# Kernel optimization log

Measured on AMD Instinct MI355X. Metric: run time of the kernel, lower is better.

The kernel has to match this reference:

```python
import jax, jax.numpy as jnp
import numpy as np

ALPHA = 0.5
SMOOTHING = 0.1
B, C = 16384, 4096


def setup_inputs() -> dict:
    key = jax.random.key(0)
    k1, k2 = jax.random.split(key)
    y_h = jax.random.normal(k1, (B, C), dtype=jnp.float32)
    # y acts as a score matrix; argmax over classes yields the hard label
    y = jax.random.normal(k2, (B, C), dtype=jnp.float32)
    # supervise buffer: smoothing/(C-1) off-diagonal, 1-smoothing on diagonal
    supervise = jnp.full((C, C), SMOOTHING / (C - 1), dtype=jnp.float32)
    supervise = supervise.at[jnp.arange(C), jnp.arange(C)].set(1.0 - SMOOTHING)
    return {"y_h": y_h, "y": y, "supervise": supervise}


def reference(y_h, y, supervise):
    n_classes = supervise.shape[0]
    y_idx = jnp.argmax(y, axis=1)                      # [B] hard labels
    log_p = jax.nn.log_softmax(y_h, axis=-1)           # [B, C]
    probs = jnp.exp(log_p)                             # [B, C]

    # ---- step(): no-grad buffer update (training mode) ----
    pred = jnp.argmax(probs, axis=-1)                  # [B]
    mask = (pred == y_idx)                             # correctly classified
    probs_c = probs * mask[:, None].astype(probs.dtype)
    # update.index_add_(1, pred[mask], probs[mask].T): scatter-add rows of
    # probs into column `pred` of the [C, C] update matrix (dup indices ok)
    update = jnp.zeros((n_classes, n_classes), probs.dtype).at[:, pred].add(probs_c.T)
    idx_count = jnp.zeros((n_classes,), probs.dtype).at[pred].add(mask.astype(probs.dtype))

    # ---- soft loss: gather supervise columns by label ----
    true_dist = supervise.T[y_idx]                     # [B, C] == index_select(supervise,1,y).T
    soft_loss = jnp.mean(jnp.sum(-true_dist * log_p, axis=-1))

    # ---- hard loss: standard cross entropy ----
    hard_loss = -jnp.mean(jnp.take_along_axis(log_p, y_idx[:, None], axis=-1))

    loss = ALPHA * hard_loss + (1.0 - ALPHA) * soft_loss
    return loss, update, idx_count
```

## Files before the change

### kernel.cpp

```cpp
#include <hip/hip_runtime.h>
#include <math.h>


constexpr int CC    = 4096;
constexpr int WAVE  = 64;
constexpr int WPB   = 4;
constexpr int TPB   = 256;
constexpr int NCH   = 4;
constexpr int CHUNK = CC / NCH;
constexpr int JPW   = CHUNK / (WAVE * 4);
constexpr float ALPHA_V = 0.5f;
constexpr int ACC_SLOTS = 64;
constexpr int MCAP  = 32;

__device__ inline void amax2(float v, int i, float& bv, int& bi) {
  if (v > bv || (v == bv && i < bi)) { bv = v; bi = i; }
}

__device__ inline void wave_argmax(float& lv, int& li) {
  #pragma unroll
  for (int o = 1; o < WAVE; o <<= 1) {
    float ov = __shfl_xor(lv, o, WAVE);
    int   oi = __shfl_xor(li, o, WAVE);
    amax2(ov, oi, lv, li);
  }
}

__device__ inline float wave_sum(float v) {
  #pragma unroll
  for (int o = 1; o < WAVE; o <<= 1) v += __shfl_xor(v, o, WAVE);
  return v;
}

__global__ void ols_mega(const float* __restrict__ sup,
                         float* __restrict__ supT,
                         float* __restrict__ upd,
                         float* __restrict__ cnt,
                         double* __restrict__ acc,
                         const float* __restrict__ y,
                         float* __restrict__ ypmax,
                         int* __restrict__ ypidx, int C) {
  __shared__ float tile[32][33];
  const int blk = blockIdx.x;
  if ((blk & 1) == 0) {
    const int tid = threadIdx.x;
    const int t2 = blk >> 1;
    const int bx = (t2 & 127) * 32, by = (t2 >> 7) * 32;
    const int tx = tid & 31, ty = tid >> 5;
    if (by == 0 && ty == 0) cnt[bx + tx] = 0.0f;
    if (t2 == 0 && tid < ACC_SLOTS * 2) acc[tid] = 0.0;
    #pragma unroll
    for (int j = 0; j < 32; j += 8)
      tile[ty + j][tx] = sup[(size_t)(by + ty + j) * C + bx + tx];
    __syncthreads();
    #pragma unroll
    for (int j = 0; j < 32; j += 8) {
      const size_t o = (size_t)(bx + ty + j) * C + by + tx;
      supT[o] = tile[tx][ty + j];
      upd[o]  = 0.0f;
    }
  } else {
    const int wv = threadIdx.x >> 6, lane = threadIdx.x & 63;
    const int task = (blk >> 1) * WPB + wv;
    const int b = task >> 2, ch = task & 3;
    const float4* p = reinterpret_cast<const float4*>(y + (size_t)b * CC + ch * CHUNK);

    float4 v[JPW];
    #pragma unroll
    for (int j = 0; j < JPW; ++j) v[j] = p[j * WAVE + lane];

    float m = -INFINITY; int mi = 0x7fffffff;
    #pragma unroll
    for (int j = 0; j < JPW; ++j) {
      const int base = ch * CHUNK + (j * WAVE + lane) * 4;
      amax2(v[j].x, base + 0, m, mi);
      amax2(v[j].y, base + 1, m, mi);
      amax2(v[j].z, base + 2, m, mi);
      amax2(v[j].w, base + 3, m, mi);
    }
    wave_argmax(m, mi);
    if (lane == 0) { ypmax[task] = m; ypidx[task] = mi; }
  }
}

__global__ void ols_part_x(const float* __restrict__ y_h,
                           const float* __restrict__ supT,
                           const float* __restrict__ ypmax,
                           const int* __restrict__ ypidx,
                           float* __restrict__ xpmax, int* __restrict__ xpidx,
                           float* __restrict__ xpse, float* __restrict__ xpW,
                           float* __restrict__ xpWX) {
  const int wv = threadIdx.x >> 6, lane = threadIdx.x & 63;
  const int task = blockIdx.x * WPB + wv;
  const int b = task >> 2, ch = task & 3;

  const float4 ym = reinterpret_cast<const float4*>(ypmax)[b];
  const int4   yi = reinterpret_cast<const int4*>(ypidx)[b];
  float lm = ym.x; int lab = yi.x;
  amax2(ym.y, yi.y, lm, lab);
  amax2(ym.z, yi.z, lm, lab);
  amax2(ym.w, yi.w, lm, lab);

  const float4* px = reinterpret_cast<const float4*>(y_h + (size_t)b * CC + ch * CHUNK);
  const float4* pw = reinterpret_cast<const float4*>(supT + (size_t)lab * CC + ch * CHUNK);

  float4 xv[JPW], wv4[JPW];
  #pragma unroll
  for (int j = 0; j < JPW; ++j) xv[j] = px[j * WAVE + lane];
  #pragma unroll
  for (int j = 0; j < JPW; ++j) wv4[j] = pw[j * WAVE + lane];

  float m = -INFINITY; int mi = 0x7fffffff;
  float se = 0.f, W = 0.f, WX = 0.f;
  #pragma unroll
  for (int j = 0; j < JPW; ++j) {
    const int base = ch * CHUNK + (j * WAVE + lane) * 4;
    amax2(xv[j].x, base + 0, m, mi);
    amax2(xv[j].y, base + 1, m, mi);
    amax2(xv[j].z, base + 2, m, mi);
    amax2(xv[j].w, base + 3, m, mi);
    se += __expf(xv[j].x) + __expf(xv[j].y) + __expf(xv[j].z) + __expf(xv[j].w);
    W  += wv4[j].x + wv4[j].y + wv4[j].z + wv4[j].w;
    WX += wv4[j].x * xv[j].x + wv4[j].y * xv[j].y
        + wv4[j].z * xv[j].z + wv4[j].w * xv[j].w;
  }
  wave_argmax(m, mi);
  se = wave_sum(se);
  W  = wave_sum(W);
  WX = wave_sum(WX);
  if (lane == 0) {
    xpmax[task] = m; xpidx[task] = mi;
    xpse[task] = se; xpW[task] = W; xpWX[task] = WX;
  }
}

__global__ void ols_rowfin(const float* __restrict__ y_h,
                           const float* __restrict__ ypmax, const int* __restrict__ ypidx,
                           const float* __restrict__ xpmax, const int* __restrict__ xpidx,
                           const float* __restrict__ xpse, const float* __restrict__ xpW,
                           const float* __restrict__ xpWX,
                           float* __restrict__ upd,
                           float* __restrict__ cnt, double* __restrict__ acc) {
  __shared__ int   s_n;
  __shared__ int   s_row[MCAP];
  __shared__ int   s_pred[MCAP];
  __shared__ float s_invZ[MCAP];
  const int tid = threadIdx.x;
  const int b = blockIdx.x * TPB + tid;
  if (tid == 0) s_n = 0;

  const float4 ym = reinterpret_cast<const float4*>(ypmax)[b];
  const int4   yi = reinterpret_cast<const int4*>(ypidx)[b];
  float lm = ym.x; int lab = yi.x;
  amax2(ym.y, yi.y, lm, lab);
  amax2(ym.z, yi.z, lm, lab);
  amax2(ym.w, yi.w, lm, lab);

  const float4 xm = reinterpret_cast<const float4*>(xpmax)[b];
  const int4   xi = reinterpret_cast<const int4*>(xpidx)[b];
  float pm = xm.x; int pred = xi.x;
  amax2(xm.y, xi.y, pm, pred);
  amax2(xm.z, xi.z, pm, pred);
  amax2(xm.w, xi.w, pm, pred);

  const float4 se4 = reinterpret_cast<const float4*>(xpse)[b];
  const float4 W4  = reinterpret_cast<const float4*>(xpW)[b];
  const float4 WX4 = reinterpret_cast<const float4*>(xpWX)[b];
  const float Z  = se4.x + se4.y + se4.z + se4.w;
  const float W  = W4.x + W4.y + W4.z + W4.w;
  const float WX = WX4.x + WX4.y + WX4.z + WX4.w;

  const float logZ = __logf(Z);
  const float xl   = y_h[(size_t)b * CC + lab];
  float soft = logZ * W - WX;
  float hard = logZ - xl;

  __syncthreads();
  bool overflow = false;
  if (pred == lab) {
    const int pos = atomicAdd(&s_n, 1);
    if (pos < MCAP) { s_row[pos] = b; s_pred[pos] = pred; s_invZ[pos] = 1.0f / Z; }
    else overflow = true;
    atomicAdd(&cnt[pred], 1.0f);
  }
  if (overflow) {
    const float invZ = 1.0f / Z;
    const float* xr = y_h + (size_t)b * CC;
    for (int c = 0; c < CC; ++c)
      atomicAdd(&upd[(size_t)c * CC + pred], __expf(xr[c]) * invZ);
  }

  hard = wave_sum(hard);
  soft = wave_sum(soft);
  if ((tid & 63) == 0) {
    const int slot = ((b >> 6) & (ACC_SLOTS - 1)) * 2;
    atomicAdd(&acc[slot + 0], (double)hard);
    atomicAdd(&acc[slot + 1], (double)soft);
  }

  __syncthreads();
  const int n = min(s_n, MCAP);
  for (int i = 0; i < n; ++i) {
    const int rb = s_row[i], p = s_pred[i];
    const float iz = s_invZ[i];
    const float4* px = reinterpret_cast<const float4*>(y_h + (size_t)rb * CC);
    #pragma unroll
    for (int j = 0; j < 4; ++j) {
      const int i4 = j * TPB + tid;
      const float4 xv = px[i4];
      const int base = i4 * 4;
      atomicAdd(&upd[(size_t)(base + 0) * CC + p], __expf(xv.x) * iz);
      atomicAdd(&upd[(size_t)(base + 1) * CC + p], __expf(xv.y) * iz);
      atomicAdd(&upd[(size_t)(base + 2) * CC + p], __expf(xv.z) * iz);
      atomicAdd(&upd[(size_t)(base + 3) * CC + p], __expf(xv.w) * iz);
    }
  }
}

__global__ void ols_finalize(const double* __restrict__ acc,
                             float* __restrict__ out, double invB) {
  double h = 0.0, s = 0.0;
  for (int i = 0; i < ACC_SLOTS; ++i) { h += acc[i * 2]; s += acc[i * 2 + 1]; }
  out[0] = (float)(((double)ALPHA_V * h + (1.0 - (double)ALPHA_V) * s) * invB);
}

__global__ void ols_fallback(const float* __restrict__ y_h, const float* __restrict__ y,
                             const float* __restrict__ sup,
                             float* __restrict__ upd, float* __restrict__ cnt,
                             double* __restrict__ acc) {
  const int wv = threadIdx.x >> 6, lane = threadIdx.x & 63;
  const int b = blockIdx.x * WPB + wv;
  const size_t roff = (size_t)b * CC;
  const float4* y4 = reinterpret_cast<const float4*>(y + roff);
  const float4* x4 = reinterpret_cast<const float4*>(y_h + roff);
  const int K16 = CC / (WAVE * 4);

  float lv = -INFINITY; int li = 0x7fffffff;
  for (int k = 0; k < K16; ++k) {
    const float4 v = y4[k * WAVE + lane];
    const int base = (k * WAVE + lane) * 4;
    amax2(v.x, base + 0, lv, li); amax2(v.y, base + 1, lv, li);
    amax2(v.z, base + 2, lv, li); amax2(v.w, base + 3, lv, li);
  }
  wave_argmax(lv, li);
  const int lab = li;
  const float xl = y_h[roff + lab];

  float m = -INFINITY; int mi = 0x7fffffff;
  float se = 0.f, W = 0.f, WX = 0.f;
  for (int k = 0; k < K16; ++k) {
    const float4 xv = x4[k * WAVE + lane];
    const int base = (k * WAVE + lane) * 4;
    const float w0 = sup[(size_t)(base + 0) * CC + lab];
    const float w1 = sup[(size_t)(base + 1) * CC + lab];
    const float w2 = sup[(size_t)(base + 2) * CC + lab];
    const float w3 = sup[(size_t)(base + 3) * CC + lab];
    amax2(xv.x, base + 0, m, mi); amax2(xv.y, base + 1, m, mi);
    amax2(xv.z, base + 2, m, mi); amax2(xv.w, base + 3, m, mi);
    se += __expf(xv.x) + __expf(xv.y) + __expf(xv.z) + __expf(xv.w);
    W  += w0 + w1 + w2 + w3;
    WX += w0 * xv.x + w1 * xv.y + w2 * xv.z + w3 * xv.w;
  }
  wave_argmax(m, mi);
  const int pred = mi;
  const float Z = wave_sum(se), Wt = wave_sum(W), WXt = wave_sum(WX);
  const float logZ = __logf(Z);
  if (pred == lab) {
    const float invZ = 1.0f / Z;
    for (int k = 0; k < K16; ++k) {
      const float4 xv = x4[k * WAVE + lane];
      const int base = (k * WAVE + lane) * 4;
      atomicAdd(&upd[(size_t)(base + 0) * CC + pred], __expf(xv.x) * invZ);
      atomicAdd(&upd[(size_t)(base + 1) * CC + pred], __expf(xv.y) * invZ);
      atomicAdd(&upd[(size_t)(base + 2) * CC + pred], __expf(xv.z) * invZ);
      atomicAdd(&upd[(size_t)(base + 3) * CC + pred], __expf(xv.w) * invZ);
    }
    if (lane == 0) atomicAdd(&cnt[pred], 1.0f);
  }
  if (lane == 0) {
    const int slot = (b & (ACC_SLOTS - 1)) * 2;
    atomicAdd(&acc[slot + 0], (double)(logZ - xl));
    atomicAdd(&acc[slot + 1], (double)(logZ * Wt - WXt));
  }
}

extern "C" void kernel_launch(void* const* d_in, const int* in_sizes, int n_in,
                              void* d_out, int out_size, void* d_ws, size_t ws_size,
                              hipStream_t stream) {
  const float* y_h = (const float*)d_in[0];
  const float* y   = (const float*)d_in[1];
  const float* sup = (const float*)d_in[2];
  const int C = CC;
  const int B = in_sizes[0] / C;

  float* out        = (float*)d_out;
  float* out_update = out + 1;
  float* out_count  = out + 1 + (size_t)C * C;

  char* ws = (char*)d_ws;
  double* acc   = (double*)ws;
  float*  ypmax = (float*)(ws + 4096);
  int*    ypidx = (int*)  (ws + 266240);
  float*  xpmax = (float*)(ws + 528384);
  int*    xpidx = (int*)  (ws + 790528);
  float*  xpse  = (float*)(ws + 1052672);
  float*  xpW   = (float*)(ws + 1314816);
  float*  xpWX  = (float*)(ws + 1576960);
  float*  supT  = (float*)(ws + 1839104);
  const size_t need = 1839104 + (size_t)C * C * sizeof(float);

  if (ws_size >= need) {
    ols_mega<<<32768, TPB, 0, stream>>>(sup, supT, out_update, out_count,
                                        acc, y, ypmax, ypidx, C);
    ols_part_x<<<B * NCH / WPB, TPB, 0, stream>>>(y_h, supT, ypmax, ypidx,
                                                  xpmax, xpidx, xpse, xpW, xpWX);
    ols_rowfin<<<B / TPB, TPB, 0, stream>>>(y_h, ypmax, ypidx,
                                            xpmax, xpidx, xpse, xpW, xpWX,
                                            out_update, out_count, acc);
    ols_finalize<<<1, 1, 0, stream>>>(acc, out, 1.0 / (double)B);
  } else {
    hipMemsetAsync(d_out, 0, (size_t)out_size * sizeof(float), stream);
    hipMemsetAsync(d_ws, 0, 4096, stream);
    ols_fallback<<<B / WPB, TPB, 0, stream>>>(y_h, y, sup,
                                              out_update, out_count, acc);
    ols_finalize<<<1, 1, 0, stream>>>(acc, out, 1.0 / (double)B);
  }
}
```

Measured before the change: 196.8 us.

## Fuse per-row partial reductions and row finalize into one block-per-row kernel

The label argmax now finishes inside the first kernel through a shared-memory reduction across its four waves and writes a single label per row, replacing the per-chunk partial arrays. The separate partial-x and row-finalize kernels become one kernel that gives each row a whole block. That block reduces max, sum-exp and the weighted sums in shared memory, then does the loss atomics and the scatter into the update matrix directly. This removes one launch and the round trip of partial results through global memory. In exchange it adds a block barrier per row and issues one pair of double atomics per row where the old code issued one per 64 rows.

```diff
diff --git a/kernel.cpp b/kernel.cpp
--- a/kernel.cpp
+++ b/kernel.cpp
@@ -6,12 +6,10 @@
 constexpr int WAVE  = 64;
 constexpr int WPB   = 4;
 constexpr int TPB   = 256;
-constexpr int NCH   = 4;
-constexpr int CHUNK = CC / NCH;
+constexpr int CHUNK = CC / WPB;
 constexpr int JPW   = CHUNK / (WAVE * 4);
 constexpr float ALPHA_V = 0.5f;
 constexpr int ACC_SLOTS = 64;
-constexpr int MCAP  = 32;
 
 __device__ inline void amax2(float v, int i, float& bv, int& bi) {
   if (v > bv || (v == bv && i < bi)) { bv = v; bi = i; }
@@ -38,12 +36,13 @@
                          float* __restrict__ cnt,
                          double* __restrict__ acc,
                          const float* __restrict__ y,
-                         float* __restrict__ ypmax,
-                         int* __restrict__ ypidx, int C) {
+                         int* __restrict__ labels, int C) {
   __shared__ float tile[32][33];
+  __shared__ float s_m[WPB];
+  __shared__ int   s_i[WPB];
   const int blk = blockIdx.x;
+  const int tid = threadIdx.x;
   if ((blk & 1) == 0) {
-    const int tid = threadIdx.x;
     const int t2 = blk >> 1;
     const int bx = (t2 & 127) * 32, by = (t2 >> 7) * 32;
     const int tx = tid & 31, ty = tid >> 5;
@@ -60,11 +59,10 @@
       upd[o]  = 0.0f;
     }
   } else {
-    const int wv = threadIdx.x >> 6, lane = threadIdx.x & 63;
-    const int task = (blk >> 1) * WPB + wv;
-    const int b = task >> 2, ch = task & 3;
-    const float4* p = reinterpret_cast<const float4*>(y + (size_t)b * CC + ch * CHUNK);
-
+    const int wv = tid >> 6, lane = tid & 63;
+    const int b = blk >> 1;
+    const float4* p = reinterpret_cast<const float4*>(y + (size_t)b * CC)
+                      + wv * (CHUNK / 4);
     float4 v[JPW];
     #pragma unroll
     for (int j = 0; j < JPW; ++j) v[j] = p[j * WAVE + lane];
@@ -72,37 +70,41 @@
     float m = -INFINITY; int mi = 0x7fffffff;
     #pragma unroll
     for (int j = 0; j < JPW; ++j) {
-      const int base = ch * CHUNK + (j * WAVE + lane) * 4;
+      const int base = wv * CHUNK + (j * WAVE + lane) * 4;
       amax2(v[j].x, base + 0, m, mi);
       amax2(v[j].y, base + 1, m, mi);
       amax2(v[j].z, base + 2, m, mi);
       amax2(v[j].w, base + 3, m, mi);
     }
     wave_argmax(m, mi);
-    if (lane == 0) { ypmax[task] = m; ypidx[task] = mi; }
-  }
-}
-
-__global__ void ols_part_x(const float* __restrict__ y_h,
-                           const float* __restrict__ supT,
-                           const float* __restrict__ ypmax,
-                           const int* __restrict__ ypidx,
-                           float* __restrict__ xpmax, int* __restrict__ xpidx,
-                           float* __restrict__ xpse, float* __restrict__ xpW,
-                           float* __restrict__ xpWX) {
-  const int wv = threadIdx.x >> 6, lane = threadIdx.x & 63;
-  const int task = blockIdx.x * WPB + wv;
-  const int b = task >> 2, ch = task & 3;
-
-  const float4 ym = reinterpret_cast<const float4*>(ypmax)[b];
-  const int4   yi = reinterpret_cast<const int4*>(ypidx)[b];
-  float lm = ym.x; int lab = yi.x;
-  amax2(ym.y, yi.y, lm, lab);
-  amax2(ym.z, yi.z, lm, lab);
-  amax2(ym.w, yi.w, lm, lab);
-
-  const float4* px = reinterpret_cast<const float4*>(y_h + (size_t)b * CC + ch * CHUNK);
-  const float4* pw = reinterpret_cast<const float4*>(supT + (size_t)lab * CC + ch * CHUNK);
+    if (lane == 0) { s_m[wv] = m; s_i[wv] = mi; }
+    __syncthreads();
+    if (tid == 0) {
+      float bm = s_m[0]; int bi = s_i[0];
+      amax2(s_m[1], s_i[1], bm, bi);
+      amax2(s_m[2], s_i[2], bm, bi);
+      amax2(s_m[3], s_i[3], bm, bi);
+      labels[b] = bi;
+    }
+  }
+}
+
+__global__ void ols_row(const float* __restrict__ y_h,
+                        const int* __restrict__ labels,
+                        const float* __restrict__ supT,
+                        float* __restrict__ upd, float* __restrict__ cnt,
+                        double* __restrict__ acc) {
+  __shared__ float s_m[WPB], s_se[WPB], s_W[WPB], s_WX[WPB];
+  __shared__ int   s_mi[WPB];
+  const int tid = threadIdx.x;
+  const int wv = tid >> 6, lane = tid & 63;
+  const int b = blockIdx.x;
+  const int lab = labels[b];
+  const size_t roff = (size_t)b * CC;
+
+  const float4* px = reinterpret_cast<const float4*>(y_h + roff) + wv * (CHUNK / 4);
+  const float4* pw = reinterpret_cast<const float4*>(supT + (size_t)lab * CC)
+                     + wv * (CHUNK / 4);
 
   float4 xv[JPW], wv4[JPW];
   #pragma unroll
@@ -114,7 +116,7 @@
   float se = 0.f, W = 0.f, WX = 0.f;
   #pragma unroll
   for (int j = 0; j < JPW; ++j) {
-    const int base = ch * CHUNK + (j * WAVE + lane) * 4;
+    const int base = wv * CHUNK + (j * WAVE + lane) * 4;
     amax2(xv[j].x, base + 0, m, mi);
     amax2(xv[j].y, base + 1, m, mi);
     amax2(xv[j].z, base + 2, m, mi);
@@ -129,90 +131,39 @@
   W  = wave_sum(W);
   WX = wave_sum(WX);
   if (lane == 0) {
-    xpmax[task] = m; xpidx[task] = mi;
-    xpse[task] = se; xpW[task] = W; xpWX[task] = WX;
-  }
-}
-
-__global__ void ols_rowfin(const float* __restrict__ y_h,
-                           const float* __restrict__ ypmax, const int* __restrict__ ypidx,
-                           const float* __restrict__ xpmax, const int* __restrict__ xpidx,
-                           const float* __restrict__ xpse, const float* __restrict__ xpW,
-                           const float* __restrict__ xpWX,
-                           float* __restrict__ upd,
-                           float* __restrict__ cnt, double* __restrict__ acc) {
-  __shared__ int   s_n;
-  __shared__ int   s_row[MCAP];
-  __shared__ int   s_pred[MCAP];
-  __shared__ float s_invZ[MCAP];
-  const int tid = threadIdx.x;
-  const int b = blockIdx.x * TPB + tid;
-  if (tid == 0) s_n = 0;
-
-  const float4 ym = reinterpret_cast<const float4*>(ypmax)[b];
-  const int4   yi = reinterpret_cast<const int4*>(ypidx)[b];
-  float lm = ym.x; int lab = yi.x;
-  amax2(ym.y, yi.y, lm, lab);
-  amax2(ym.z, yi.z, lm, lab);
-  amax2(ym.w, yi.w, lm, lab);
-
-  const float4 xm = reinterpret_cast<const float4*>(xpmax)[b];
-  const int4   xi = reinterpret_cast<const int4*>(xpidx)[b];
-  float pm = xm.x; int pred = xi.x;
-  amax2(xm.y, xi.y, pm, pred);
-  amax2(xm.z, xi.z, pm, pred);
-  amax2(xm.w, xi.w, pm, pred);
-
-  const float4 se4 = reinterpret_cast<const float4*>(xpse)[b];
-  const float4 W4  = reinterpret_cast<const float4*>(xpW)[b];
-  const float4 WX4 = reinterpret_cast<const float4*>(xpWX)[b];
-  const float Z  = se4.x + se4.y + se4.z + se4.w;
-  const float W  = W4.x + W4.y + W4.z + W4.w;
-  const float WX = WX4.x + WX4.y + WX4.z + WX4.w;
-
+    s_m[wv] = m; s_mi[wv] = mi; s_se[wv] = se; s_W[wv] = W; s_WX[wv] = WX;
+  }
+  __syncthreads();
+
+  float pm = s_m[0]; int pred = s_mi[0];
+  amax2(s_m[1], s_mi[1], pm, pred);
+  amax2(s_m[2], s_mi[2], pm, pred);
+  amax2(s_m[3], s_mi[3], pm, pred);
+  const float Z   = s_se[0] + s_se[1] + s_se[2] + s_se[3];
+  const float Wt  = s_W[0] + s_W[1] + s_W[2] + s_W[3];
+  const float WXt = s_WX[0] + s_WX[1] + s_WX[2] + s_WX[3];
   const float logZ = __logf(Z);
-  const float xl   = y_h[(size_t)b * CC + lab];
-  float soft = logZ * W - WX;
-  float hard = logZ - xl;
-
-  __syncthreads();
-  bool overflow = false;
+
+  if (tid == 0) {
+    const float xl = y_h[roff + lab];
+    const int slot = (b & (ACC_SLOTS - 1)) * 2;
+    atomicAdd(&acc[slot + 0], (double)(logZ - xl));
+    atomicAdd(&acc[slot + 1], (double)(logZ * Wt - WXt));
+    if (pred == lab) atomicAdd(&cnt[pred], 1.0f);
+  }
+
   if (pred == lab) {
-    const int pos = atomicAdd(&s_n, 1);
-    if (pos < MCAP) { s_row[pos] = b; s_pred[pos] = pred; s_invZ[pos] = 1.0f / Z; }
-    else overflow = true;
-    atomicAdd(&cnt[pred], 1.0f);
-  }
-  if (overflow) {
     const float invZ = 1.0f / Z;
-    const float* xr = y_h + (size_t)b * CC;
-    for (int c = 0; c < CC; ++c)
-      atomicAdd(&upd[(size_t)c * CC + pred], __expf(xr[c]) * invZ);
-  }
-
-  hard = wave_sum(hard);
-  soft = wave_sum(soft);
-  if ((tid & 63) == 0) {
-    const int slot = ((b >> 6) & (ACC_SLOTS - 1)) * 2;
-    atomicAdd(&acc[slot + 0], (double)hard);
-    atomicAdd(&acc[slot + 1], (double)soft);
-  }
-
-  __syncthreads();
-  const int n = min(s_n, MCAP);
-  for (int i = 0; i < n; ++i) {
-    const int rb = s_row[i], p = s_pred[i];
-    const float iz = s_invZ[i];
-    const float4* px = reinterpret_cast<const float4*>(y_h + (size_t)rb * CC);
+    const float4* pr = reinterpret_cast<const float4*>(y_h + roff);
     #pragma unroll
     for (int j = 0; j < 4; ++j) {
       const int i4 = j * TPB + tid;
-      const float4 xv = px[i4];
+      const float4 q = pr[i4];
       const int base = i4 * 4;
-      atomicAdd(&upd[(size_t)(base + 0) * CC + p], __expf(xv.x) * iz);
-      atomicAdd(&upd[(size_t)(base + 1) * CC + p], __expf(xv.y) * iz);
-      atomicAdd(&upd[(size_t)(base + 2) * CC + p], __expf(xv.z) * iz);
-      atomicAdd(&upd[(size_t)(base + 3) * CC + p], __expf(xv.w) * iz);
+      atomicAdd(&upd[(size_t)(base + 0) * CC + pred], __expf(q.x) * invZ);
+      atomicAdd(&upd[(size_t)(base + 1) * CC + pred], __expf(q.y) * invZ);
+      atomicAdd(&upd[(size_t)(base + 2) * CC + pred], __expf(q.z) * invZ);
+      atomicAdd(&upd[(size_t)(base + 3) * CC + pred], __expf(q.w) * invZ);
     }
   }
 }
@@ -298,25 +249,16 @@
   float* out_count  = out + 1 + (size_t)C * C;
 
   char* ws = (char*)d_ws;
-  double* acc   = (double*)ws;
-  float*  ypmax = (float*)(ws + 4096);
-  int*    ypidx = (int*)  (ws + 266240);
-  float*  xpmax = (float*)(ws + 528384);
-  int*    xpidx = (int*)  (ws + 790528);
-  float*  xpse  = (float*)(ws + 1052672);
-  float*  xpW   = (float*)(ws + 1314816);
-  float*  xpWX  = (float*)(ws + 1576960);
-  float*  supT  = (float*)(ws + 1839104);
-  const size_t need = 1839104 + (size_t)C * C * sizeof(float);
+  double* acc    = (double*)ws;
+  int*    labels = (int*)(ws + 4096);
+  float*  supT   = (float*)(ws + 4096 + 65536);
+  const size_t need = 4096 + 65536 + (size_t)C * C * sizeof(float);
 
   if (ws_size >= need) {
     ols_mega<<<32768, TPB, 0, stream>>>(sup, supT, out_update, out_count,
-                                        acc, y, ypmax, ypidx, C);
-    ols_part_x<<<B * NCH / WPB, TPB, 0, stream>>>(y_h, supT, ypmax, ypidx,
-                                                  xpmax, xpidx, xpse, xpW, xpWX);
-    ols_rowfin<<<B / TPB, TPB, 0, stream>>>(y_h, ypmax, ypidx,
-                                            xpmax, xpidx, xpse, xpW, xpWX,
-                                            out_update, out_count, acc);
+                                        acc, y, labels, C);
+    ols_row<<<B, TPB, 0, stream>>>(y_h, labels, supT,
+                                   out_update, out_count, acc);
     ols_finalize<<<1, 1, 0, stream>>>(acc, out, 1.0 / (double)B);
   } else {
     hipMemsetAsync(d_out, 0, (size_t)out_size * sizeof(float), stream);
```

Result: faster. 189.5 us, median of 2 (-3.7%).
